# Optimization experiments

Hardware: AMD Instinct MI355X
Metric: run time of the kernel (lower is better)

## Reference

```python
import jax, jax.numpy as jnp
import numpy as np

RF, US, MGC, FS, NS, NL = 1024, 200, 60, 64, 4, 10  # receptive field, upsample, mgc, filters, stacks, wavenet layers
SCALE = 0.70710678118


def setup_inputs() -> dict:
    key = jax.random.key(0)
    ks = jax.random.split(key, 16)
    F = 8
    N = F * US
    def n(k, shape, s=0.05):
        return jax.random.normal(k, shape, dtype=jnp.float32) * s
    return {
        "mgc": n(ks[0], (F, MGC), 1.0),
        "noise": n(ks[1], (N + RF,), 1.0),
        "cond_w": n(ks[2], (MGC * US, MGC)),          # conditioning Linear(60 -> 12000)
        "cond_b": n(ks[3], (MGC * US,)),
        "conv0_w": n(ks[4], (NS, 3, FS, 1, 2), 0.3),    # layer 0: in_ch=1, [input,gate,residual]
        "convs_w": n(ks[5], (NS, NL - 1, 3, FS, FS, 2), 0.08),
        "conv_b": n(ks[6], (NS, NL, 3, FS)),
        "ccw": n(ks[7], (NS, NL, 2, FS, MGC)),          # cond_input / cond_gate linear weights
        "ccb": n(ks[8], (NS, NL, 2, FS)),
        "pre_w": n(ks[9], (NS, 256, FS)),
        "pre_b": n(ks[10], (NS, 256)),
        "mean_w": n(ks[11], (NS, 1, 256)),
        "mean_b": n(ks[12], (NS, 1)),
        "std_w": n(ks[13], (NS, 1, 256)),
        "std_b": n(ks[14], (NS, 1)),
    }


def _cond_conv(x, cond, w, b, cw, cb):
    # x: [N, C, L]; kernel-2 stride-2 conv expressed as a reshape + einsum
    Nb, C, L = x.shape
    xr = x.reshape(Nb, C, L // 2, 2)
    inp = jnp.einsum('ncls,ocs->nol', xr, w[0]) + b[0][None, :, None]
    gate = jnp.einsum('ncls,ocs->nol', xr, w[1]) + b[1][None, :, None]
    res = jnp.einsum('ncls,ocs->nol', xr, w[2]) + b[2][None, :, None]
    ic = (cond @ cw[0].T + cb[0])[:, :, None]
    gc = (cond @ cw[1].T + cb[1])[:, :, None]
    return (jnp.tanh(inp + ic) * jax.nn.sigmoid(gate + gc) + res) * SCALE


def reference(mgc, noise, cond_w, cond_b, conv0_w, convs_w, conv_b, ccw, ccb,
              pre_w, pre_b, mean_w, mean_b, std_w, std_b):
    F = mgc.shape[0]
    N = F * US
    # conditioning: Linear(60 -> 60*200) + tanh, reshaped to one 60-dim vector per sample
    cond = jnp.tanh(mgc @ cond_w.T + cond_b).reshape(N, MGC)
    prepend = noise[:RF]
    prev_x = noise
    win_idx = jnp.arange(N)[:, None] + jnp.arange(RF)[None, :]  # strided-window gather
    tails = []
    mean = logvar = None
    for s in range(NS):
        x = prev_x[win_idx][:, None, :]  # [N, 1, RF]
        for l in range(NL):
            w = conv0_w[s] if l == 0 else convs_w[s, l - 1]
            x = _cond_conv(x, cond, w, conv_b[s, l], ccw[s, l], ccb[s, l])
        pre = jax.nn.relu(x[:, :, 0] @ pre_w[s].T + pre_b[s])   # [N, 256]
        mean = pre @ mean_w[s].T + mean_b[s]                    # [N, 1]
        logvar = pre @ std_w[s].T + std_b[s]                    # [N, 1]
        eps = prev_x[RF:].reshape(N, 1)
        new = eps * jnp.exp(0.5 * logvar) + mean
        tails.append(jax.lax.stop_gradient(new[-RF:]))
        if s != NS - 1:
            prev_x = jnp.concatenate([prepend, new.reshape(-1)])
        else:
            prev_x = new
    return prev_x, mean, logvar, jnp.stack(tails)
```

## Files before the change

### kernel.cpp

```cpp
#include <hip/hip_runtime.h>
#include <hip/hip_fp16.h>

#define RF    1024
#define USZ   200
#define NWIN  1600
#define SCALEF 0.70710678118f
#define L2E2  2.885390082f
#define L2E   1.442695041f
#define TPB   512
#define CSTR  72

typedef _Float16 f16x8 __attribute__((ext_vector_type(8)));
typedef float    f32x4 __attribute__((ext_vector_type(4)));

#if __has_builtin(__builtin_amdgcn_exp2f)
#define EXP2F(x) __builtin_amdgcn_exp2f(x)
#else
#define EXP2F(x) exp2f(x)
#endif
#if __has_builtin(__builtin_amdgcn_rcpf)
#define RCPF(x) __builtin_amdgcn_rcpf(x)
#else
#define RCPF(x) (1.0f / (x))
#endif

__device__ __forceinline__ float gatecomb(float a, float g, float rp) {
  const float u = EXP2F(a);
  const float v = EXP2F(g);
  const float num = fmaf(u, v, -v);
  const float den = (u + 1.0f) * (v + 1.0f);
  return fmaf(num * RCPF(den), SCALEF, rp);
}


__global__ void k_cond(const float* __restrict__ mgc, const float* __restrict__ cond_w,
                       const float* __restrict__ cond_b, _Float16* __restrict__ cond_h) {
  int idx = blockIdx.x * 256 + threadIdx.x;
  int n = idx >> 6, c = idx & 63;
  if (c >= 60) { cond_h[idx] = (_Float16)0.0f; return; }
  int u = n % USZ, f = n / USZ;
  float a = cond_b[u * 60 + c];
  const float* wr = cond_w + (u * 60 + c) * 60;
  const float* mr = mgc + f * 60;
#pragma unroll 10
  for (int m = 0; m < 60; ++m) a = fmaf(mr[m], wr[m], a);
  float e = EXP2F(a * L2E2);
  cond_h[idx] = (_Float16)((e - 1.0f) * RCPF(e + 1.0f));
}

__global__ void k_packB(const float* __restrict__ ccw, _Float16* __restrict__ wfrag2) {
  int idx = blockIdx.x * 256 + threadIdx.x;
  int j    = idx & 7;
  int lane = (idx >> 3) & 63;
  int ks   = (idx >> 9) & 1;
  int nt   = (idx >> 10) & 7;
  int sl   = idx >> 13;
  int jo = nt * 16 + (lane & 15);
  int c  = ks * 32 + (lane >> 4) * 8 + j;
  float v = 0.0f;
  if (c < 60) v = ccw[((sl * 2 + (jo >> 6)) * 64 + (jo & 63)) * 60 + c];
  wfrag2[idx] = (_Float16)v;
}

__global__ void k_icgc_mfma(const _Float16* __restrict__ cond_h, const _Float16* __restrict__ wfrag2,
                            const float* __restrict__ ccb, const float* __restrict__ conv_b,
                            float* __restrict__ icgc) {
  const int n0 = blockIdx.x * 32;
  const int sl = blockIdx.y;
  const int tid = threadIdx.x;
  const int wave = tid >> 6, lane = tid & 63;
  const int m16 = lane & 15, q = lane >> 4;
  for (int t = wave; t < 16; t += 4) {
    const int mt = t >> 3, nt = t & 7;
    const int jo = nt * 16 + m16;
    const float b = ccb[(sl * 2 + (jo >> 6)) * 64 + (jo & 63)]
                  + conv_b[(sl * 3 + (jo >> 6)) * 64 + (jo & 63)];
    f32x4 acc = {b, b, b, b};
    const int arow = (n0 + mt * 16 + m16) * 64 + q * 8;
    const f16x8 a0 = *(const f16x8*)(cond_h + arow);
    const f16x8 a1 = *(const f16x8*)(cond_h + arow + 32);
    const f16x8* wb = (const f16x8*)wfrag2;
    const f16x8 b0 = wb[(((sl * 8 + nt) * 2 + 0) << 6) + lane];
    const f16x8 b1 = wb[(((sl * 8 + nt) * 2 + 1) << 6) + lane];
    acc = __builtin_amdgcn_mfma_f32_16x16x32_f16(a0, b0, acc, 0, 0, 0);
    acc = __builtin_amdgcn_mfma_f32_16x16x32_f16(a1, b1, acc, 0, 0, 0);
    const float gs = (jo >= 64) ? L2E : L2E2;
#pragma unroll
    for (int r = 0; r < 4; ++r) {
      const int n = n0 + mt * 16 + q * 4 + r;
      icgc[((size_t)sl * 1600 + n) * 128 + jo] = acc[r] * gs;
    }
  }
}

__global__ void k_wcvt(const float* __restrict__ convs_w, _Float16* __restrict__ wfrag) {
  int idx = blockIdx.x * 256 + threadIdx.x;
  int j    = idx & 7;
  int lane = (idx >> 3) & 63;
  int ks   = (idx >> 9) & 3;
  int ch16 = (idx >> 11) & 3;
  int t    = idx >> 13;
  int gate = t % 3, sl = t / 3;
  int o  = ch16 * 16 + (lane & 15);
  int kk = ks * 32 + (lane >> 4) * 8 + j;
  int s2 = kk >> 6, c = kk & 63;
  const float gs = (gate == 0) ? L2E2 : ((gate == 1) ? L2E : SCALEF);
  wfrag[idx] = (_Float16)(convs_w[(((sl * 3 + gate) * 64 + o) * 64 + c) * 2 + s2] * gs);
}

__global__ void k_pwt(const float* __restrict__ pre_w, float* __restrict__ pwT) {
  int idx = blockIdx.x * 256 + threadIdx.x;
  int k = idx & 255, o = (idx >> 8) & 63, s = idx >> 14;
  pwT[idx] = pre_w[(s * 256 + k) * 64 + o];
}

__global__ void k_prefix(const float* __restrict__ noise, float* __restrict__ pxA,
                         float* __restrict__ pxB) {
  int i = blockIdx.x * 256 + threadIdx.x;
  float v = noise[i];
  pxA[i] = v; pxB[i] = v;
}

#define SMEM_BYTES 79184

__device__ __forceinline__ void run_mfma_tiles(
    const _Float16* __restrict__ ain, _Float16* __restrict__ aout, float* __restrict__ x64f,
    const f16x8 bfr[3][4], float bi, float bg, float br,
    int mt_lo, int mt_hi, int row_sub, int Lout, bool last,
    int q, int m16, int och)
{
  for (int mt = mt_lo; mt < mt_hi; mt += 2) {
    f32x4 ai = {bi, bi, bi, bi};
    f32x4 ag = {bg, bg, bg, bg};
    f32x4 ar = {br, br, br, br};
#pragma unroll
    for (int ks = 0; ks < 4; ++ks) {
      const int row = 2 * (mt * 16 + m16) + (ks >> 1) - row_sub;
      const f16x8 af = *(const f16x8*)(ain + row * CSTR + (ks & 1) * 32 + q * 8);
      ai = __builtin_amdgcn_mfma_f32_16x16x32_f16(af, bfr[0][ks], ai, 0, 0, 0);
      ag = __builtin_amdgcn_mfma_f32_16x16x32_f16(af, bfr[1][ks], ag, 0, 0, 0);
      ar = __builtin_amdgcn_mfma_f32_16x16x32_f16(af, bfr[2][ks], ar, 0, 0, 0);
    }
#pragma unroll
    for (int r = 0; r < 4; ++r) {
      const int p = mt * 16 + q * 4 + r;
      const float val = gatecomb(ai[r], ag[r], ar[r]);
      if (last) { if (p == 0) x64f[och] = val; }
      else if (p < Lout) aout[p * CSTR + och] = (_Float16)val;
    }
  }
}

__launch_bounds__(TPB, 4)
__global__ void k_window(int s, const float* __restrict__ px, float* __restrict__ ptail,
                         float* __restrict__ out,
                         const float* __restrict__ icgc, const float* __restrict__ conv_b,
                         const float* __restrict__ conv0_w, const _Float16* __restrict__ wfrag,
                         const float* __restrict__ pwT, const float* __restrict__ pre_b,
                         const float* __restrict__ mean_w, const float* __restrict__ mean_b,
                         const float* __restrict__ std_w, const float* __restrict__ std_b) {
  extern __shared__ char smem[];
  _Float16* bufA = (_Float16*)smem;
  _Float16* bufB = (_Float16*)(smem + 36864);
  float*    xw   = (float*)(smem + 73728);
  float*    x64f = (float*)(smem + 77840);
  float*    pre  = (float*)(smem + 78096);
  float*    red  = (float*)(smem + 79120);

  const int n = blockIdx.x;
  const int tid = threadIdx.x;
  const int wave = tid >> 6, lane = tid & 63;
  const int q = lane >> 4, m16 = lane & 15;
  const int ch16 = wave & 3, mstart = wave >> 2;
  const int och = ch16 * 16 + m16;

  for (int i = tid; i < 1025; i += TPB) xw[i] = px[n + i];

  const int b0 = ((s * 10 + 0) * 1600 + n) * 128;
  const float l0bi = icgc[b0 + lane];
  const float l0bg = icgc[b0 + 64 + lane];
  const float l0br = conv_b[((s * 10 + 0) * 3 + 2) * 64 + lane] * SCALEF;
  const float wi0 = conv0_w[((s * 3 + 0) * 64 + lane) * 2 + 0] * L2E2;
  const float wi1 = conv0_w[((s * 3 + 0) * 64 + lane) * 2 + 1] * L2E2;
  const float wg0 = conv0_w[((s * 3 + 1) * 64 + lane) * 2 + 0] * L2E;
  const float wg1 = conv0_w[((s * 3 + 1) * 64 + lane) * 2 + 1] * L2E;
  const float wr0 = conv0_w[((s * 3 + 2) * 64 + lane) * 2 + 0] * SCALEF;
  const float wr1 = conv0_w[((s * 3 + 2) * 64 + lane) * 2 + 1] * SCALEF;

  f16x8 bfr1[3][4];
  {
    const f16x8* wb = (const f16x8*)(wfrag + (size_t)(s * 9) * 24576);
#pragma unroll
    for (int g = 0; g < 3; ++g)
#pragma unroll
      for (int ks = 0; ks < 4; ++ks)
        bfr1[g][ks] = wb[(((g * 4 + ch16) * 4 + ks) << 6) + lane];
  }
  const int base1 = ((s * 10 + 1) * 1600 + n) * 128;
  const float bi1 = icgc[base1 + och];
  const float bg1 = icgc[base1 + 64 + och];
  const float br1 = conv_b[((s * 10 + 1) * 3 + 2) * 64 + och] * SCALEF;

  __syncthreads();

#pragma unroll 1
  for (int p = wave; p < 256; p += 8) {
    const float x0 = xw[2 * p], x1 = xw[2 * p + 1];
    const float vi = fmaf(x1, wi1, fmaf(x0, wi0, l0bi));
    const float vg = fmaf(x1, wg1, fmaf(x0, wg0, l0bg));
    const float vr = fmaf(x1, wr1, fmaf(x0, wr0, l0br));
    bufA[p * CSTR + lane] = (_Float16)gatecomb(vi, vg, vr);
  }
  __syncthreads();

  run_mfma_tiles(bufA, bufB, x64f, bfr1, bi1, bg1, br1, mstart, 8, 0, 256, false, q, m16, och);
  __syncthreads();

#pragma unroll 1
  for (int p = wave; p < 256; p += 8) {
    const int pg = 256 + p;
    const float x0 = xw[2 * pg], x1 = xw[2 * pg + 1];
    const float vi = fmaf(x1, wi1, fmaf(x0, wi0, l0bi));
    const float vg = fmaf(x1, wg1, fmaf(x0, wg0, l0bg));
    const float vr = fmaf(x1, wr1, fmaf(x0, wr0, l0br));
    bufA[p * CSTR + lane] = (_Float16)gatecomb(vi, vg, vr);
  }
  __syncthreads();

  run_mfma_tiles(bufA, bufB, x64f, bfr1, bi1, bg1, br1, 8 + mstart, 16, 256, 256, false, q, m16, och);
  __syncthreads();

#pragma unroll 1
  for (int l = 2; l <= 9; ++l) {
    const int Lout = 512 >> l;
    const int mtiles = (Lout + 15) >> 4;
    const _Float16* ain = (l & 1) ? bufA : bufB;
    _Float16* aout      = (l & 1) ? bufB : bufA;
    f16x8 bfr[3][4];
    const f16x8* wb = (const f16x8*)(wfrag + (size_t)(s * 9 + (l - 1)) * 24576);
#pragma unroll
    for (int g = 0; g < 3; ++g)
#pragma unroll
      for (int ks = 0; ks < 4; ++ks)
        bfr[g][ks] = wb[(((g * 4 + ch16) * 4 + ks) << 6) + lane];
    const int base = ((s * 10 + l) * 1600 + n) * 128;
    run_mfma_tiles(ain, aout, x64f, bfr,
                   icgc[base + och], icgc[base + 64 + och],
                   conv_b[((s * 10 + l) * 3 + 2) * 64 + och] * SCALEF,
                   mstart, mtiles, 0, Lout, l == 9, q, m16, och);
    __syncthreads();
  }

  if (tid < 256) {
    const int k = tid;
    float a = pre_b[s * 256 + k];
#pragma unroll 8
    for (int oo = 0; oo < 64; ++oo)
      a = fmaf(x64f[oo], pwT[(s * 64 + oo) * 256 + k], a);
    pre[k] = fmaxf(a, 0.0f);
  }
  __syncthreads();
  {
    float pm = 0.0f, pv = 0.0f;
    if (tid < 256) {
      float pk = pre[tid];
      pm = pk * mean_w[s * 256 + tid];
      pv = pk * std_w[s * 256 + tid];
    }
    for (int off = 32; off >= 1; off >>= 1) {
      pm += __shfl_down(pm, off, 64);
      pv += __shfl_down(pv, off, 64);
    }
    if (lane == 0) { red[wave] = pm; red[8 + wave] = pv; }
  }
  __syncthreads();
  if (tid == 0) {
    float m = mean_b[s], lv = std_b[s];
#pragma unroll
    for (int w2 = 0; w2 < 8; ++w2) { m += red[w2]; lv += red[8 + w2]; }
    float eps = xw[1024];
    float nv = eps * __expf(0.5f * lv) + m;
    if (s == 3) { out[n] = nv; out[1600 + n] = m; out[3200 + n] = lv; }
    else ptail[n] = nv;
    if (n >= 576) out[4800 + s * 1024 + (n - 576)] = nv;
  }
}

extern "C" void kernel_launch(void* const* d_in, const int* in_sizes, int n_in,
                              void* d_out, int out_size, void* d_ws, size_t ws_size,
                              hipStream_t stream) {
  (void)in_sizes; (void)n_in; (void)out_size; (void)ws_size;
  const float* mgc     = (const float*)d_in[0];
  const float* noise   = (const float*)d_in[1];
  const float* cond_w  = (const float*)d_in[2];
  const float* cond_b  = (const float*)d_in[3];
  const float* conv0_w = (const float*)d_in[4];
  const float* convs_w = (const float*)d_in[5];
  const float* conv_b  = (const float*)d_in[6];
  const float* ccw     = (const float*)d_in[7];
  const float* ccb     = (const float*)d_in[8];
  const float* pre_w   = (const float*)d_in[9];
  const float* pre_b   = (const float*)d_in[10];
  const float* mean_w  = (const float*)d_in[11];
  const float* mean_b  = (const float*)d_in[12];
  const float* std_w   = (const float*)d_in[13];
  const float* std_b   = (const float*)d_in[14];
  float* out = (float*)d_out;

  char* ws = (char*)d_ws;
  float*    icgc   = (float*)ws;
  float*    pxA    = (float*)(ws + 32768000);
  float*    pxB    = (float*)(ws + 32778496);
  float*    pwT    = (float*)(ws + 32788992);
  _Float16* wfrag  = (_Float16*)(ws + 33051136);
  _Float16* wfrag2 = (_Float16*)(ws + 34820608);
  _Float16* cond_h = (_Float16*)(ws + 35475968);

  k_cond<<<400, 256, 0, stream>>>(mgc, cond_w, cond_b, cond_h);
  k_packB<<<1280, 256, 0, stream>>>(ccw, wfrag2);
  k_icgc_mfma<<<dim3(50, 40), 256, 0, stream>>>(cond_h, wfrag2, ccb, conv_b, icgc);
  k_wcvt<<<3456, 256, 0, stream>>>(convs_w, wfrag);
  k_pwt<<<256, 256, 0, stream>>>(pre_w, pwT);
  k_prefix<<<4, 256, 0, stream>>>(noise, pxA, pxB);

  (void)hipFuncSetAttribute((const void*)k_window,
                            hipFuncAttributeMaxDynamicSharedMemorySize, SMEM_BYTES);

  for (int s = 0; s < 4; ++s) {
    const float* pin = (s == 0) ? noise : (s == 1 ? pxA : (s == 2 ? pxB : pxA));
    float* pt = (s == 0) ? (pxA + 1024) : (s == 1 ? (pxB + 1024) : (s == 2 ? (pxA + 1024) : nullptr));
    k_window<<<NWIN, TPB, SMEM_BYTES, stream>>>(s, pin, pt, out, icgc, conv_b, conv0_w,
                                                wfrag, pwT, pre_b, mean_w, mean_b, std_w, std_b);
  }
}
```

Before: 539.2 us.

## Stream early WaveNet layers in chunks to shrink LDS footprint and raise occupancy

Layers 1–3 are now computed in small chunks: layer 0 produces 64 positions at a time into a 64-row scratch buffer, and layers 2–3 are interleaved over two halves. This lets the full-size ping-pong buffer plus a small scratch replace two full-size buffers, cutting shared memory from about 79 KB to about 46 KB per block. Launch bounds are raised from 4 to 6 so more blocks can be resident per CU. In exchange there are more barriers, weight fragments are reloaded from global memory for each chunk, and the input window is read straight from global memory instead of being staged in shared memory.

```diff
diff --git a/kernel.cpp b/kernel.cpp
--- a/kernel.cpp
+++ b/kernel.cpp
@@ -121,37 +121,53 @@
   pxA[i] = v; pxB[i] = v;
 }
 
-#define SMEM_BYTES 79184
-
-__device__ __forceinline__ void run_mfma_tiles(
-    const _Float16* __restrict__ ain, _Float16* __restrict__ aout, float* __restrict__ x64f,
-    const f16x8 bfr[3][4], float bi, float bg, float br,
-    int mt_lo, int mt_hi, int row_sub, int Lout, bool last,
-    int q, int m16, int och)
+#define SMEM_BYTES 46080
+
+__device__ __forceinline__ void tiles(
+    const _Float16* __restrict__ inb, int in_row0,
+    _Float16* __restrict__ outb, int out_row0, float* __restrict__ x64f,
+    const _Float16* __restrict__ wfl,
+    const float* __restrict__ icgc, const float* __restrict__ conv_b,
+    int sl, int n, int nt, int Lout, bool last,
+    int mstart, int q, int m16, int och, int lane, int ch16)
 {
-  for (int mt = mt_lo; mt < mt_hi; mt += 2) {
+  if (mstart >= nt) return;
+  const int base = (sl * 1600 + n) * 128;
+  const float bi = icgc[base + och];
+  const float bg = icgc[base + 64 + och];
+  const float br = conv_b[(sl * 3 + 2) * 64 + och] * SCALEF;
+  f16x8 bfr[3][4];
+  const f16x8* wb = (const f16x8*)wfl;
+#pragma unroll
+  for (int g = 0; g < 3; ++g)
+#pragma unroll
+    for (int ks = 0; ks < 4; ++ks)
+      bfr[g][ks] = wb[(((g * 4 + ch16) * 4 + ks) << 6) + lane];
+
+#pragma unroll 1
+  for (int mt = mstart; mt < nt; mt += 2) {
     f32x4 ai = {bi, bi, bi, bi};
     f32x4 ag = {bg, bg, bg, bg};
     f32x4 ar = {br, br, br, br};
 #pragma unroll
     for (int ks = 0; ks < 4; ++ks) {
-      const int row = 2 * (mt * 16 + m16) + (ks >> 1) - row_sub;
-      const f16x8 af = *(const f16x8*)(ain + row * CSTR + (ks & 1) * 32 + q * 8);
+      const int row = in_row0 + 2 * (mt * 16 + m16) + (ks >> 1);
+      const f16x8 af = *(const f16x8*)(inb + row * CSTR + (ks & 1) * 32 + q * 8);
       ai = __builtin_amdgcn_mfma_f32_16x16x32_f16(af, bfr[0][ks], ai, 0, 0, 0);
       ag = __builtin_amdgcn_mfma_f32_16x16x32_f16(af, bfr[1][ks], ag, 0, 0, 0);
       ar = __builtin_amdgcn_mfma_f32_16x16x32_f16(af, bfr[2][ks], ar, 0, 0, 0);
     }
-#pragma unroll
+#pragma unroll 2
     for (int r = 0; r < 4; ++r) {
       const int p = mt * 16 + q * 4 + r;
       const float val = gatecomb(ai[r], ag[r], ar[r]);
       if (last) { if (p == 0) x64f[och] = val; }
-      else if (p < Lout) aout[p * CSTR + och] = (_Float16)val;
-    }
-  }
-}
-
-__launch_bounds__(TPB, 4)
+      else if (p < Lout) outb[(out_row0 + p) * CSTR + och] = (_Float16)val;
+    }
+  }
+}
+
+__launch_bounds__(TPB, 6)
 __global__ void k_window(int s, const float* __restrict__ px, float* __restrict__ ptail,
                          float* __restrict__ out,
                          const float* __restrict__ icgc, const float* __restrict__ conv_b,
@@ -160,12 +176,11 @@
                          const float* __restrict__ mean_w, const float* __restrict__ mean_b,
                          const float* __restrict__ std_w, const float* __restrict__ std_b) {
   extern __shared__ char smem[];
-  _Float16* bufA = (_Float16*)smem;
-  _Float16* bufB = (_Float16*)(smem + 36864);
-  float*    xw   = (float*)(smem + 73728);
-  float*    x64f = (float*)(smem + 77840);
-  float*    pre  = (float*)(smem + 78096);
-  float*    red  = (float*)(smem + 79120);
+  _Float16* X    = (_Float16*)smem;
+  _Float16* Y    = (_Float16*)(smem + 36864);
+  float*    x64f = (float*)(smem + 9216);
+  float*    pre  = (float*)(smem + 9472);
+  float*    red  = (float*)(smem + 10496);
 
   const int n = blockIdx.x;
   const int tid = threadIdx.x;
@@ -173,81 +188,57 @@
   const int q = lane >> 4, m16 = lane & 15;
   const int ch16 = wave & 3, mstart = wave >> 2;
   const int och = ch16 * 16 + m16;
-
-  for (int i = tid; i < 1025; i += TPB) xw[i] = px[n + i];
-
-  const int b0 = ((s * 10 + 0) * 1600 + n) * 128;
-  const float l0bi = icgc[b0 + lane];
-  const float l0bg = icgc[b0 + 64 + lane];
-  const float l0br = conv_b[((s * 10 + 0) * 3 + 2) * 64 + lane] * SCALEF;
-  const float wi0 = conv0_w[((s * 3 + 0) * 64 + lane) * 2 + 0] * L2E2;
-  const float wi1 = conv0_w[((s * 3 + 0) * 64 + lane) * 2 + 1] * L2E2;
-  const float wg0 = conv0_w[((s * 3 + 1) * 64 + lane) * 2 + 0] * L2E;
-  const float wg1 = conv0_w[((s * 3 + 1) * 64 + lane) * 2 + 1] * L2E;
-  const float wr0 = conv0_w[((s * 3 + 2) * 64 + lane) * 2 + 0] * SCALEF;
-  const float wr1 = conv0_w[((s * 3 + 2) * 64 + lane) * 2 + 1] * SCALEF;
-
-  f16x8 bfr1[3][4];
-  {
-    const f16x8* wb = (const f16x8*)(wfrag + (size_t)(s * 9) * 24576);
-#pragma unroll
-    for (int g = 0; g < 3; ++g)
-#pragma unroll
-      for (int ks = 0; ks < 4; ++ks)
-        bfr1[g][ks] = wb[(((g * 4 + ch16) * 4 + ks) << 6) + lane];
-  }
-  const int base1 = ((s * 10 + 1) * 1600 + n) * 128;
-  const float bi1 = icgc[base1 + och];
-  const float bg1 = icgc[base1 + 64 + och];
-  const float br1 = conv_b[((s * 10 + 1) * 3 + 2) * 64 + och] * SCALEF;
-
-  __syncthreads();
-
-#pragma unroll 1
-  for (int p = wave; p < 256; p += 8) {
-    const float x0 = xw[2 * p], x1 = xw[2 * p + 1];
-    const float vi = fmaf(x1, wi1, fmaf(x0, wi0, l0bi));
-    const float vg = fmaf(x1, wg1, fmaf(x0, wg0, l0bg));
-    const float vr = fmaf(x1, wr1, fmaf(x0, wr0, l0br));
-    bufA[p * CSTR + lane] = (_Float16)gatecomb(vi, vg, vr);
-  }
-  __syncthreads();
-
-  run_mfma_tiles(bufA, bufB, x64f, bfr1, bi1, bg1, br1, mstart, 8, 0, 256, false, q, m16, och);
-  __syncthreads();
-
-#pragma unroll 1
-  for (int p = wave; p < 256; p += 8) {
-    const int pg = 256 + p;
-    const float x0 = xw[2 * pg], x1 = xw[2 * pg + 1];
-    const float vi = fmaf(x1, wi1, fmaf(x0, wi0, l0bi));
-    const float vg = fmaf(x1, wg1, fmaf(x0, wg0, l0bg));
-    const float vr = fmaf(x1, wr1, fmaf(x0, wr0, l0br));
-    bufA[p * CSTR + lane] = (_Float16)gatecomb(vi, vg, vr);
-  }
-  __syncthreads();
-
-  run_mfma_tiles(bufA, bufB, x64f, bfr1, bi1, bg1, br1, 8 + mstart, 16, 256, 256, false, q, m16, och);
-  __syncthreads();
-
-#pragma unroll 1
-  for (int l = 2; l <= 9; ++l) {
+  const int s10 = s * 10;
+  const _Float16* wf1 = wfrag + (size_t)(s * 9) * 24576;
+
+#pragma unroll 1
+  for (int c = 0; c < 8; ++c) {
+    {
+      const int b0 = (s10 * 1600 + n) * 128;
+      const float l0bi = icgc[b0 + lane];
+      const float l0bg = icgc[b0 + 64 + lane];
+      const float l0br = conv_b[(s10 * 3 + 2) * 64 + lane] * SCALEF;
+      const float wi0 = conv0_w[((s * 3 + 0) * 64 + lane) * 2 + 0] * L2E2;
+      const float wi1 = conv0_w[((s * 3 + 0) * 64 + lane) * 2 + 1] * L2E2;
+      const float wg0 = conv0_w[((s * 3 + 1) * 64 + lane) * 2 + 0] * L2E;
+      const float wg1 = conv0_w[((s * 3 + 1) * 64 + lane) * 2 + 1] * L2E;
+      const float wr0 = conv0_w[((s * 3 + 2) * 64 + lane) * 2 + 0] * SCALEF;
+      const float wr1 = conv0_w[((s * 3 + 2) * 64 + lane) * 2 + 1] * SCALEF;
+#pragma unroll 1
+      for (int r = wave; r < 64; r += 8) {
+        const int pg = c * 64 + r;
+        const float x0 = px[n + 2 * pg];
+        const float x1 = px[n + 2 * pg + 1];
+        const float vi = fmaf(x1, wi1, fmaf(x0, wi0, l0bi));
+        const float vg = fmaf(x1, wg1, fmaf(x0, wg0, l0bg));
+        const float vr = fmaf(x1, wr1, fmaf(x0, wr0, l0br));
+        Y[r * CSTR + lane] = (_Float16)gatecomb(vi, vg, vr);
+      }
+    }
+    __syncthreads();
+    tiles(Y, 0, X, 32 * c, x64f, wf1, icgc, conv_b, s10 + 1, n,
+          2, 32, false, mstart, q, m16, och, lane, ch16);
+    __syncthreads();
+  }
+
+#pragma unroll 1
+  for (int c = 0; c < 2; ++c) {
+    tiles(X, 128 * c, Y, 0, x64f, wfrag + (size_t)(s * 9 + 1) * 24576, icgc, conv_b,
+          s10 + 2, n, 4, 64, false, mstart, q, m16, och, lane, ch16);
+    __syncthreads();
+    tiles(Y, 0, X, 32 * c, x64f, wfrag + (size_t)(s * 9 + 2) * 24576, icgc, conv_b,
+          s10 + 3, n, 2, 32, false, mstart, q, m16, och, lane, ch16);
+    __syncthreads();
+  }
+#pragma unroll 1
+  for (int l = 4; l <= 9; ++l) {
     const int Lout = 512 >> l;
-    const int mtiles = (Lout + 15) >> 4;
-    const _Float16* ain = (l & 1) ? bufA : bufB;
-    _Float16* aout      = (l & 1) ? bufB : bufA;
-    f16x8 bfr[3][4];
-    const f16x8* wb = (const f16x8*)(wfrag + (size_t)(s * 9 + (l - 1)) * 24576);
-#pragma unroll
-    for (int g = 0; g < 3; ++g)
-#pragma unroll
-      for (int ks = 0; ks < 4; ++ks)
-        bfr[g][ks] = wb[(((g * 4 + ch16) * 4 + ks) << 6) + lane];
-    const int base = ((s * 10 + l) * 1600 + n) * 128;
-    run_mfma_tiles(ain, aout, x64f, bfr,
-                   icgc[base + och], icgc[base + 64 + och],
-                   conv_b[((s * 10 + l) * 3 + 2) * 64 + och] * SCALEF,
-                   mstart, mtiles, 0, Lout, l == 9, q, m16, och);
+    const int nt = (Lout + 15) >> 4;
+    const bool evenl = (l & 1) == 0;
+    const _Float16* inb = evenl ? X : Y;
+    _Float16* outb      = evenl ? Y : X;
+    tiles(inb, 0, outb, 0, x64f, wfrag + (size_t)(s * 9 + (l - 1)) * 24576, icgc, conv_b,
+          s10 + l, n, nt, Lout, l == 9, mstart, q, m16, och, lane, ch16);
     __syncthreads();
   }
 
@@ -278,7 +269,7 @@
     float m = mean_b[s], lv = std_b[s];
 #pragma unroll
     for (int w2 = 0; w2 < 8; ++w2) { m += red[w2]; lv += red[8 + w2]; }
-    float eps = xw[1024];
+    float eps = px[n + RF];
     float nv = eps * __expf(0.5f * lv) + m;
     if (s == 3) { out[n] = nv; out[1600 + n] = m; out[3200 + n] = lv; }
     else ptail[n] = nv;
```

Measured after the change: 1.211 ms. 125% more time.

## Run tail WaveNet layers and output head on a single wave without block barriers

Applied to the files above, without the earlier changes.

Layers 5-9, whose outputs are 16 or fewer rows, now run on wave 0 alone. That wave loops over all four 16-channel groups and reloads their weight fragments from global memory. The other seven waves exit early, and the pre/mean/std head becomes a single-wave computation using register accumulators and shuffle reductions, with no shared-memory reduction. This removes five block barriers and idle waves in the tiny layers, but serializes their MFMA work onto one wave and adds global weight loads.

```diff
diff --git a/kernel.cpp b/kernel.cpp
--- a/kernel.cpp
+++ b/kernel.cpp
@@ -23,6 +23,8 @@
 #else
 #define RCPF(x) (1.0f / (x))
 #endif
+
+#define MFMA16(a, b, c) __builtin_amdgcn_mfma_f32_16x16x32_f16((a), (b), (c), 0, 0, 0)
 
 __device__ __forceinline__ float gatecomb(float a, float g, float rp) {
   const float u = EXP2F(a);
@@ -82,8 +84,8 @@
     const f16x8* wb = (const f16x8*)wfrag2;
     const f16x8 b0 = wb[(((sl * 8 + nt) * 2 + 0) << 6) + lane];
     const f16x8 b1 = wb[(((sl * 8 + nt) * 2 + 1) << 6) + lane];
-    acc = __builtin_amdgcn_mfma_f32_16x16x32_f16(a0, b0, acc, 0, 0, 0);
-    acc = __builtin_amdgcn_mfma_f32_16x16x32_f16(a1, b1, acc, 0, 0, 0);
+    acc = MFMA16(a0, b0, acc);
+    acc = MFMA16(a1, b1, acc);
     const float gs = (jo >= 64) ? L2E : L2E2;
 #pragma unroll
     for (int r = 0; r < 4; ++r) {
@@ -121,12 +123,12 @@
   pxA[i] = v; pxB[i] = v;
 }
 
-#define SMEM_BYTES 79184
+#define SMEM_BYTES 78096
 
 __device__ __forceinline__ void run_mfma_tiles(
-    const _Float16* __restrict__ ain, _Float16* __restrict__ aout, float* __restrict__ x64f,
+    const _Float16* __restrict__ ain, _Float16* __restrict__ aout,
     const f16x8 bfr[3][4], float bi, float bg, float br,
-    int mt_lo, int mt_hi, int row_sub, int Lout, bool last,
+    int mt_lo, int mt_hi, int row_sub, int Lout,
     int q, int m16, int och)
 {
   for (int mt = mt_lo; mt < mt_hi; mt += 2) {
@@ -137,16 +139,15 @@
     for (int ks = 0; ks < 4; ++ks) {
       const int row = 2 * (mt * 16 + m16) + (ks >> 1) - row_sub;
       const f16x8 af = *(const f16x8*)(ain + row * CSTR + (ks & 1) * 32 + q * 8);
-      ai = __builtin_amdgcn_mfma_f32_16x16x32_f16(af, bfr[0][ks], ai, 0, 0, 0);
-      ag = __builtin_amdgcn_mfma_f32_16x16x32_f16(af, bfr[1][ks], ag, 0, 0, 0);
-      ar = __builtin_amdgcn_mfma_f32_16x16x32_f16(af, bfr[2][ks], ar, 0, 0, 0);
+      ai = MFMA16(af, bfr[0][ks], ai);
+      ag = MFMA16(af, bfr[1][ks], ag);
+      ar = MFMA16(af, bfr[2][ks], ar);
     }
-#pragma unroll
+#pragma unroll 2
     for (int r = 0; r < 4; ++r) {
       const int p = mt * 16 + q * 4 + r;
       const float val = gatecomb(ai[r], ag[r], ar[r]);
-      if (last) { if (p == 0) x64f[och] = val; }
-      else if (p < Lout) aout[p * CSTR + och] = (_Float16)val;
+      if (p < Lout) aout[p * CSTR + och] = (_Float16)val;
     }
   }
 }
@@ -164,8 +165,6 @@
   _Float16* bufB = (_Float16*)(smem + 36864);
   float*    xw   = (float*)(smem + 73728);
   float*    x64f = (float*)(smem + 77840);
-  float*    pre  = (float*)(smem + 78096);
-  float*    red  = (float*)(smem + 79120);
 
   const int n = blockIdx.x;
   const int tid = threadIdx.x;
@@ -173,13 +172,14 @@
   const int q = lane >> 4, m16 = lane & 15;
   const int ch16 = wave & 3, mstart = wave >> 2;
   const int och = ch16 * 16 + m16;
+  const int s10 = s * 10;
 
   for (int i = tid; i < 1025; i += TPB) xw[i] = px[n + i];
 
-  const int b0 = ((s * 10 + 0) * 1600 + n) * 128;
+  const int b0 = (s10 * 1600 + n) * 128;
   const float l0bi = icgc[b0 + lane];
   const float l0bg = icgc[b0 + 64 + lane];
-  const float l0br = conv_b[((s * 10 + 0) * 3 + 2) * 64 + lane] * SCALEF;
+  const float l0br = conv_b[(s10 * 3 + 2) * 64 + lane] * SCALEF;
   const float wi0 = conv0_w[((s * 3 + 0) * 64 + lane) * 2 + 0] * L2E2;
   const float wi1 = conv0_w[((s * 3 + 0) * 64 + lane) * 2 + 1] * L2E2;
   const float wg0 = conv0_w[((s * 3 + 1) * 64 + lane) * 2 + 0] * L2E;
@@ -196,10 +196,10 @@
       for (int ks = 0; ks < 4; ++ks)
         bfr1[g][ks] = wb[(((g * 4 + ch16) * 4 + ks) << 6) + lane];
   }
-  const int base1 = ((s * 10 + 1) * 1600 + n) * 128;
+  const int base1 = ((s10 + 1) * 1600 + n) * 128;
   const float bi1 = icgc[base1 + och];
   const float bg1 = icgc[base1 + 64 + och];
-  const float br1 = conv_b[((s * 10 + 1) * 3 + 2) * 64 + och] * SCALEF;
+  const float br1 = conv_b[((s10 + 1) * 3 + 2) * 64 + och] * SCALEF;
 
   __syncthreads();
 
@@ -213,7 +213,7 @@
   }
   __syncthreads();
 
-  run_mfma_tiles(bufA, bufB, x64f, bfr1, bi1, bg1, br1, mstart, 8, 0, 256, false, q, m16, och);
+  run_mfma_tiles(bufA, bufB, bfr1, bi1, bg1, br1, mstart, 8, 0, 256, q, m16, och);
   __syncthreads();
 
 #pragma unroll 1
@@ -227,13 +227,13 @@
   }
   __syncthreads();
 
-  run_mfma_tiles(bufA, bufB, x64f, bfr1, bi1, bg1, br1, 8 + mstart, 16, 256, 256, false, q, m16, och);
-  __syncthreads();
-
-#pragma unroll 1
-  for (int l = 2; l <= 9; ++l) {
+  run_mfma_tiles(bufA, bufB, bfr1, bi1, bg1, br1, 8 + mstart, 16, 256, 256, q, m16, och);
+  __syncthreads();
+
+#pragma unroll 1
+  for (int l = 2; l <= 4; ++l) {
     const int Lout = 512 >> l;
-    const int mtiles = (Lout + 15) >> 4;
+    const int nt = (Lout + 15) >> 4;
     const _Float16* ain = (l & 1) ? bufA : bufB;
     _Float16* aout      = (l & 1) ? bufB : bufA;
     f16x8 bfr[3][4];
@@ -243,43 +243,83 @@
 #pragma unroll
       for (int ks = 0; ks < 4; ++ks)
         bfr[g][ks] = wb[(((g * 4 + ch16) * 4 + ks) << 6) + lane];
-    const int base = ((s * 10 + l) * 1600 + n) * 128;
-    run_mfma_tiles(ain, aout, x64f, bfr,
+    const int base = ((s10 + l) * 1600 + n) * 128;
+    run_mfma_tiles(ain, aout, bfr,
                    icgc[base + och], icgc[base + 64 + och],
-                   conv_b[((s * 10 + l) * 3 + 2) * 64 + och] * SCALEF,
-                   mstart, mtiles, 0, Lout, l == 9, q, m16, och);
+                   conv_b[((s10 + l) * 3 + 2) * 64 + och] * SCALEF,
+                   mstart, nt, 0, Lout, q, m16, och);
     __syncthreads();
   }
 
-  if (tid < 256) {
-    const int k = tid;
-    float a = pre_b[s * 256 + k];
-#pragma unroll 8
-    for (int oo = 0; oo < 64; ++oo)
-      a = fmaf(x64f[oo], pwT[(s * 64 + oo) * 256 + k], a);
-    pre[k] = fmaxf(a, 0.0f);
-  }
-  __syncthreads();
-  {
-    float pm = 0.0f, pv = 0.0f;
-    if (tid < 256) {
-      float pk = pre[tid];
-      pm = pk * mean_w[s * 256 + tid];
-      pv = pk * std_w[s * 256 + tid];
+  if (wave != 0) return;
+
+  _Float16* pa = bufA;
+  _Float16* pb = bufB;
+#pragma unroll 1
+  for (int l = 5; l <= 9; ++l) {
+    const int Lout = 512 >> l;
+    const f16x8* wb = (const f16x8*)(wfrag + (size_t)(s * 9 + (l - 1)) * 24576);
+    const int base = ((s10 + l) * 1600 + n) * 128;
+#pragma unroll 1
+    for (int g16 = 0; g16 < 4; ++g16) {
+      const int oc = g16 * 16 + m16;
+      const float bi = icgc[base + oc];
+      const float bg = icgc[base + 64 + oc];
+      const float br = conv_b[((s10 + l) * 3 + 2) * 64 + oc] * SCALEF;
+      f32x4 ai = {bi, bi, bi, bi};
+      f32x4 ag = {bg, bg, bg, bg};
+      f32x4 ar = {br, br, br, br};
+#pragma unroll
+      for (int ks = 0; ks < 4; ++ks) {
+        const f16x8 b0 = wb[(((0 * 4 + g16) * 4 + ks) << 6) + lane];
+        const f16x8 b1 = wb[(((1 * 4 + g16) * 4 + ks) << 6) + lane];
+        const f16x8 b2 = wb[(((2 * 4 + g16) * 4 + ks) << 6) + lane];
+        const int row = 2 * m16 + (ks >> 1);
+        const f16x8 af = *(const f16x8*)(pa + row * CSTR + (ks & 1) * 32 + q * 8);
+        ai = MFMA16(af, b0, ai);
+        ag = MFMA16(af, b1, ag);
+        ar = MFMA16(af, b2, ar);
+      }
+#pragma unroll
+      for (int r = 0; r < 4; ++r) {
+        const int p = q * 4 + r;
+        const float val = gatecomb(ai[r], ag[r], ar[r]);
+        if (l == 9) { if (p == 0) x64f[oc] = val; }
+        else if (p < Lout) pb[p * CSTR + oc] = (_Float16)val;
+      }
     }
-    for (int off = 32; off >= 1; off >>= 1) {
-      pm += __shfl_down(pm, off, 64);
-      pv += __shfl_down(pv, off, 64);
-    }
-    if (lane == 0) { red[wave] = pm; red[8 + wave] = pv; }
-  }
-  __syncthreads();
-  if (tid == 0) {
-    float m = mean_b[s], lv = std_b[s];
-#pragma unroll
-    for (int w2 = 0; w2 < 8; ++w2) { m += red[w2]; lv += red[8 + w2]; }
-    float eps = xw[1024];
-    float nv = eps * __expf(0.5f * lv) + m;
+    _Float16* t = pa; pa = pb; pb = t;
+  }
+
+  float a0 = pre_b[s * 256 + lane];
+  float a1 = pre_b[s * 256 + 64 + lane];
+  float a2 = pre_b[s * 256 + 128 + lane];
+  float a3 = pre_b[s * 256 + 192 + lane];
+#pragma unroll 4
+  for (int oo = 0; oo < 64; ++oo) {
+    const float xv = x64f[oo];
+    const float* pw = pwT + (s * 64 + oo) * 256;
+    a0 = fmaf(xv, pw[lane], a0);
+    a1 = fmaf(xv, pw[64 + lane], a1);
+    a2 = fmaf(xv, pw[128 + lane], a2);
+    a3 = fmaf(xv, pw[192 + lane], a3);
+  }
+  a0 = fmaxf(a0, 0.0f); a1 = fmaxf(a1, 0.0f);
+  a2 = fmaxf(a2, 0.0f); a3 = fmaxf(a3, 0.0f);
+  float pm = a0 * mean_w[s * 256 + lane] + a1 * mean_w[s * 256 + 64 + lane]
+           + a2 * mean_w[s * 256 + 128 + lane] + a3 * mean_w[s * 256 + 192 + lane];
+  float pv = a0 * std_w[s * 256 + lane] + a1 * std_w[s * 256 + 64 + lane]
+           + a2 * std_w[s * 256 + 128 + lane] + a3 * std_w[s * 256 + 192 + lane];
+#pragma unroll
+  for (int off = 32; off >= 1; off >>= 1) {
+    pm += __shfl_down(pm, off, 64);
+    pv += __shfl_down(pv, off, 64);
+  }
+  if (lane == 0) {
+    const float m = pm + mean_b[s];
+    const float lv = pv + std_b[s];
+    const float eps = xw[1024];
+    const float nv = eps * __expf(0.5f * lv) + m;
     if (s == 3) { out[n] = nv; out[1600 + n] = m; out[3200 + n] = lv; }
     else ptail[n] = nv;
     if (n >= 576) out[4800 + s * 1024 + (n - 576)] = nv;
```

Result: slower. 754.3 us (+39.9%).
